# Performance work log

Measured on AMD Instinct MI355X. Metric: run time of the kernel, lower is better.

## Reference

```python
import jax, jax.numpy as jnp
import numpy as np

B, S, D, H = 8, 2048, 768, 12

def setup_inputs() -> dict:
    key = jax.random.key(0)
    kx, km, kk, kq, kv = jax.random.split(key, 5)
    return {
        "x": jax.random.normal(kx, (B, S, D), dtype=jnp.float32),
        "mask": jax.random.randint(km, (B, 1, S), 0, 2, dtype=jnp.int32),
        "key_weight": jax.random.normal(kk, (D, H), dtype=jnp.float32),
        "query_weight": jax.random.normal(kq, (D, H), dtype=jnp.float32),
        "value_weight": jax.random.normal(kv, (D, H), dtype=jnp.float32),
    }

def reference(x, mask, key_weight, query_weight, value_weight):
    scale = 1.0 / (key_weight.shape[-1] ** 0.5)
    k = jnp.einsum('bsd,dh->bsh', x, key_weight)
    q = jnp.einsum('bsd,dh->bsh', x, query_weight)
    v = jnp.einsum('bsd,dh->bsh', x, value_weight)
    # scores: (B, S, T) — full score matrix as in the original
    scores = jnp.einsum('bsh,bth->bst', q, k) * scale
    scores = jnp.where(mask == 0, -jnp.inf, scores)
    attn = jax.nn.softmax(scores, axis=-1)
    return jnp.einsum('bst,bth->bsh', attn, v)
```

## Files before the change

kernel.cpp:

```cpp
#include <hip/hip_runtime.h>
#include <math.h>

#define QSCALE (0.2886751345948129f * 1.4426950408889634f)

#if __has_builtin(__builtin_amdgcn_exp2f)
#define EXP2F(x) __builtin_amdgcn_exp2f(x)
#else
#define EXP2F(x) exp2f(x)
#endif

typedef __attribute__((ext_vector_type(8))) _Float16 half8;
typedef __attribute__((ext_vector_type(4))) _Float16 half4_t;
typedef __attribute__((ext_vector_type(4))) float floatx4;
typedef __attribute__((ext_vector_type(2))) unsigned int uint2v;

#define MFMA32F16(a, b, c) __builtin_amdgcn_mfma_f32_16x16x32_f16((a), (b), (c), 0, 0, 0)
#define MFMA16F16(a, b, c) __builtin_amdgcn_mfma_f32_16x16x16f16((a), (b), (c), 0, 0, 0)

static __device__ inline float bperm(float v, int addr_bytes) {
    return __int_as_float(__builtin_amdgcn_ds_bpermute(addr_bytes, __float_as_int(v)));
}

static __device__ inline float xmax16(float v) {
#if __has_builtin(__builtin_amdgcn_permlane16_swap)
    unsigned int u = __float_as_uint(v);
    uint2v r = __builtin_amdgcn_permlane16_swap(u, u, false, false);
    return fmaxf(__uint_as_float(r[0]), __uint_as_float(r[1]));
#else
    return fmaxf(v, bperm(v, ((int)(threadIdx.x & 63) ^ 16) << 2));
#endif
}
static __device__ inline float xmax32(float v) {
#if __has_builtin(__builtin_amdgcn_permlane32_swap)
    unsigned int u = __float_as_uint(v);
    uint2v r = __builtin_amdgcn_permlane32_swap(u, u, false, false);
    return fmaxf(__uint_as_float(r[0]), __uint_as_float(r[1]));
#else
    return fmaxf(v, bperm(v, ((int)(threadIdx.x & 63) ^ 32) << 2));
#endif
}

__global__ __launch_bounds__(256)
void prep(const float* __restrict__ Wq, const float* __restrict__ Wk,
          const float* __restrict__ Wv, const int* __restrict__ mask,
          _Float16* __restrict__ wfh, _Float16* __restrict__ wfl,
          int* __restrict__ dst, int* __restrict__ nvalid)
{
    const int b = blockIdx.x;
    const int tid = threadIdx.x;
    if (b < 18) {
        int t = b * 256 + tid;
        if (t >= 4608) return;
        int lane = t & 63;
        int nt   = (t >> 6) % 3;
        int ks   = t / 192;
        const float* W = (nt == 0) ? Wq : (nt == 1) ? Wk : Wv;
        const float scale = (nt == 0) ? QSCALE : 1.0f;
        int col = lane & 15;
        int q8  = lane >> 4;
        half8 hi, lo;
        #pragma unroll
        for (int j = 0; j < 8; ++j) {
            int dim = ks * 32 + q8 * 8 + j;
            float f = (col < 12) ? W[dim * 12 + col] * scale : 0.0f;
            _Float16 h = (_Float16)f;
            hi[j] = h;
            lo[j] = (_Float16)(f - (float)h);
        }
        size_t off = ((size_t)(ks * 3 + nt) * 64 + lane) * 8;
        *(half8*)(wfh + off) = hi;
        *(half8*)(wfl + off) = lo;
    } else {
        __shared__ int cnt[256];
        const int bb = b - 18;
        const int* mb = mask + bb * 2048;
        int local[8]; int c = 0;
        #pragma unroll
        for (int i = 0; i < 8; ++i) { local[i] = (mb[tid * 8 + i] != 0); c += local[i]; }
        cnt[tid] = c;
        __syncthreads();
        for (int off = 1; off < 256; off <<= 1) {
            int u = cnt[tid];
            int add = (tid >= off) ? cnt[tid - off] : 0;
            __syncthreads();
            cnt[tid] = u + add;
            __syncthreads();
        }
        int run = (tid == 0) ? 0 : cnt[tid - 1];
        int* db = dst + bb * 2048;
        #pragma unroll
        for (int i = 0; i < 8; ++i) { db[tid * 8 + i] = local[i] ? run : -1; run += local[i]; }
        if (tid == 255) nvalid[bb] = cnt[255];
    }
}

__global__ __launch_bounds__(256, 3)
void qkv_mfma(const float* __restrict__ x, const _Float16* __restrict__ wfh,
              const _Float16* __restrict__ wfl, const int* __restrict__ dst,
              _Float16* __restrict__ qA, _Float16* __restrict__ qB,
              _Float16* __restrict__ kfp, _Float16* __restrict__ vtf)
{
    __shared__ __align__(16) float cbuf[3072];
    const int tid  = threadIdx.x;
    const int lane = tid & 63;
    const int w    = tid >> 6;
    const int g    = blockIdx.x;
    const int rowbase = g * 16;
    const int m15 = lane & 15;
    const int q8  = lane >> 4;

    const float* xbase = x + (size_t)(rowbase + m15) * 768 + q8 * 8;
    const half8* WH = (const half8*)wfh;
    const half8* WL = (const half8*)wfl;

    float xv[6][8];
    #pragma unroll
    for (int s = 0; s < 6; ++s) {
        const int ks = w * 6 + s;
        *(float4*)(xv[s])     = *(const float4*)(xbase + ks * 32);
        *(float4*)(xv[s] + 4) = *(const float4*)(xbase + ks * 32 + 4);
    }

    floatx4 acc0 = {0.f, 0.f, 0.f, 0.f};
    floatx4 acc1 = acc0, acc2 = acc0;

    half8 bh[2][3], bl[2][3];
    {
        const int ks = w * 6;
        #pragma unroll
        for (int n = 0; n < 3; ++n) {
            bh[0][n] = WH[(ks * 3 + n) * 64 + lane];
            bl[0][n] = WL[(ks * 3 + n) * 64 + lane];
        }
    }

    #pragma unroll
    for (int s = 0; s < 6; ++s) {
        const int cur = s & 1, nxt = cur ^ 1;
        if (s < 5) {
            const int ksn = w * 6 + s + 1;
            #pragma unroll
            for (int n = 0; n < 3; ++n) {
                bh[nxt][n] = WH[(ksn * 3 + n) * 64 + lane];
                bl[nxt][n] = WL[(ksn * 3 + n) * 64 + lane];
            }
        }
        half8 ah, al;
        #pragma unroll
        for (int j = 0; j < 8; ++j) {
            _Float16 h = (_Float16)xv[s][j];
            ah[j] = h;
            al[j] = (_Float16)(xv[s][j] - (float)h);
        }
        acc0 = MFMA32F16(ah, bh[cur][0], acc0);
        acc1 = MFMA32F16(ah, bh[cur][1], acc1);
        acc2 = MFMA32F16(ah, bh[cur][2], acc2);
        acc0 = MFMA32F16(al, bh[cur][0], acc0);
        acc1 = MFMA32F16(al, bh[cur][1], acc1);
        acc2 = MFMA32F16(al, bh[cur][2], acc2);
        acc0 = MFMA32F16(ah, bl[cur][0], acc0);
        acc1 = MFMA32F16(ah, bl[cur][1], acc1);
        acc2 = MFMA32F16(ah, bl[cur][2], acc2);
    }

    *(floatx4*)(cbuf + ((w * 3 + 0) * 64 + lane) * 4) = acc0;
    *(floatx4*)(cbuf + ((w * 3 + 1) * 64 + lane) * 4) = acc1;
    *(floatx4*)(cbuf + ((w * 3 + 2) * 64 + lane) * 4) = acc2;
    __syncthreads();
    if (w < 3) {
        floatx4 t0 = *(const floatx4*)(cbuf + ((0 * 3 + w) * 64 + lane) * 4);
        floatx4 t1 = *(const floatx4*)(cbuf + ((1 * 3 + w) * 64 + lane) * 4);
        floatx4 t2 = *(const floatx4*)(cbuf + ((2 * 3 + w) * 64 + lane) * 4);
        floatx4 t3 = *(const floatx4*)(cbuf + ((3 * 3 + w) * 64 + lane) * 4);
        floatx4 tot = t0 + t1 + t2 + t3;
        const int col = m15;
        const int r0  = q8 * 4;
        #pragma unroll
        for (int r = 0; r < 4; ++r) {
            const int row = rowbase + r0 + r;
            const float val = tot[r];
            if (w == 0) {
                if (col < 12) {
                    size_t fb = (size_t)g * 64;
                    size_t offL = (fb + (col >> 3) * 16 + (r0 + r)) * 8 + (col & 7);
                    size_t offH = (fb + (2 + (col >> 3)) * 16 + (r0 + r)) * 8 + (col & 7);
                    _Float16 h = (_Float16)val;
                    qA[offL] = h;
                    qA[offH] = h;
                    qB[offL] = (_Float16)(val - (float)h);
                    qB[offH] = (_Float16)0.0f;
                }
            } else {
                const int d = dst[row];
                if (d >= 0) {
                    const int bb = row >> 11;
                    if (w == 1) {
                        size_t fb = ((size_t)(bb * 128 + (d >> 4))) * 64;
                        size_t offH = (fb + (col >> 3) * 16 + (d & 15)) * 8 + (col & 7);
                        size_t offL = (fb + (2 + (col >> 3)) * 16 + (d & 15)) * 8 + (col & 7);
                        if (col < 12) {
                            _Float16 h = (_Float16)val;
                            kfp[offH] = h;
                            kfp[offL] = (_Float16)(val - (float)h);
                        } else {
                            kfp[offH] = (_Float16)0.0f;
                            kfp[offL] = (_Float16)0.0f;
                        }
                    } else {
                        if (col < 12) {
                            size_t off = (((size_t)(bb * 128 + (d >> 4))) * 64
                                          + ((d & 15) >> 2) * 16 + col) * 4 + (d & 3);
                            vtf[off] = (_Float16)val;
                        } else if (col == 12) {
                            size_t off = (((size_t)(bb * 128 + (d >> 4))) * 64
                                          + ((d & 15) >> 2) * 16 + 12) * 4 + (d & 3);
                            vtf[off] = (_Float16)1.0f;
                        }
                    }
                }
            }
        }
    }
}

__global__ __launch_bounds__(256)
void attn(const _Float16* __restrict__ qAf, const _Float16* __restrict__ qBf,
          const _Float16* __restrict__ kfp, const _Float16* __restrict__ vtf,
          const int* __restrict__ nvalid, float* __restrict__ out)
{
    __shared__ float cm[256];
    __shared__ __align__(16) floatx4 co[256];
    const int tid  = threadIdx.x;
    const int lane = tid & 63;
    const int w    = tid >> 6;
    const int bb   = blockIdx.x & 7;
    const int gl   = blockIdx.x >> 3;
    const int g0   = bb * 128 + gl;
    const int m15  = lane & 15;

    const half8 qA0 = *(const half8*)(qAf + ((size_t)g0 * 64 + lane) * 8);
    const half8 qB0 = *(const half8*)(qBf + ((size_t)g0 * 64 + lane) * 8);

    const half8* KP = (const half8*)kfp + (size_t)bb * 128 * 64;
    const half4_t* VT = (const half4_t*)vtf + (size_t)bb * 128 * 64;

    const int nv = nvalid[bb];
    const int nt = (nv + 15) >> 4;

    float m0 = -INFINITY;
    floatx4 o0 = {0.f, 0.f, 0.f, 0.f};

    int t = w;
    half8 kp, kp2;
    half4_t va, va2;
    if (t < nt)     { kp  = KP[t * 64 + lane];       va  = VT[t * 64 + lane]; }
    if (t + 4 < nt) { kp2 = KP[(t + 4) * 64 + lane]; va2 = VT[(t + 4) * 64 + lane]; }
    for (; t < nt; t += 8) {
        const int t2 = t + 4;
        const bool has2 = (t2 < nt);
        half8 nkp, nkp2; half4_t nva, nva2;
        if (t + 8 < nt)  { nkp  = KP[(t + 8) * 64 + lane];  nva  = VT[(t + 8) * 64 + lane]; }
        if (t + 12 < nt) { nkp2 = KP[(t + 12) * 64 + lane]; nva2 = VT[(t + 12) * 64 + lane]; }
        if (t == nt - 1) {
            const int kb = t * 16;
            if (kb + m15 >= nv) {
                #pragma unroll
                for (int j = 0; j < 8; ++j) kp[j] = (_Float16)0.0f;
            }
            const int kv = kb + (lane >> 4) * 4;
            #pragma unroll
            for (int j = 0; j < 4; ++j)
                if (kv + j >= nv) va[j] = (_Float16)0.0f;
        }
        if (has2 && t2 == nt - 1) {
            const int kb = t2 * 16;
            if (kb + m15 >= nv) {
                #pragma unroll
                for (int j = 0; j < 8; ++j) kp2[j] = (_Float16)0.0f;
            }
            const int kv = kb + (lane >> 4) * 4;
            #pragma unroll
            for (int j = 0; j < 4; ++j)
                if (kv + j >= nv) va2[j] = (_Float16)0.0f;
        }
        const floatx4 z = {0.f, 0.f, 0.f, 0.f};
        floatx4 s0a = MFMA32F16(kp, qA0, z);
        floatx4 s0b = MFMA32F16(kp, qB0, z);
        floatx4 s1 = z;
        if (has2) {
            floatx4 s1a = MFMA32F16(kp2, qA0, z);
            floatx4 s1b = MFMA32F16(kp2, qB0, z);
            s1 = s1a + s1b;
        }
        floatx4 s0 = s0a + s0b;
        float pm = fmaxf(fmaxf(s0.x, s0.y), fmaxf(s0.z, s0.w));
        if (has2) {
            float pm1 = fmaxf(fmaxf(s1.x, s1.y), fmaxf(s1.z, s1.w));
            pm = fmaxf(pm, pm1);
        }
        pm = xmax16(pm);
        pm = xmax32(pm);
        float mref;
        if (__all(pm <= m0)) {
            mref = m0;
        } else {
            float mnew = fmaxf(m0, pm);
            float corr = EXP2F(m0 - mnew);
            o0.x *= corr; o0.y *= corr; o0.z *= corr; o0.w *= corr;
            m0 = mnew; mref = mnew;
        }
        half4_t pb;
        pb[0] = (_Float16)EXP2F(s0.x - mref);
        pb[1] = (_Float16)EXP2F(s0.y - mref);
        pb[2] = (_Float16)EXP2F(s0.z - mref);
        pb[3] = (_Float16)EXP2F(s0.w - mref);
        o0 = MFMA16F16(va, pb, o0);
        if (has2) {
            half4_t pb2;
            pb2[0] = (_Float16)EXP2F(s1.x - mref);
            pb2[1] = (_Float16)EXP2F(s1.y - mref);
            pb2[2] = (_Float16)EXP2F(s1.z - mref);
            pb2[3] = (_Float16)EXP2F(s1.w - mref);
            o0 = MFMA16F16(va2, pb2, o0);
        }
        kp = nkp; va = nva; kp2 = nkp2; va2 = nva2;
    }

    cm[w * 64 + lane] = m0;
    co[w * 64 + lane] = o0;
    __syncthreads();
    if (w == 0) {
        float gm = -INFINITY;
        #pragma unroll
        for (int w2 = 0; w2 < 4; ++w2) gm = fmaxf(gm, cm[w2 * 64 + lane]);
        floatx4 O = {0.f, 0.f, 0.f, 0.f};
        #pragma unroll
        for (int w2 = 0; w2 < 4; ++w2) {
            float f = EXP2F(cm[w2 * 64 + lane] - gm);
            floatx4 ow = co[w2 * 64 + lane];
            O.x += ow.x * f; O.y += ow.y * f; O.z += ow.z * f; O.w += ow.w * f;
        }
        float L = bperm(O.x, (48 + m15) << 2);
        float inv = 1.0f / L;
        if ((lane >> 4) < 3) {
            float4 ov = make_float4(O.x * inv, O.y * inv, O.z * inv, O.w * inv);
            *(float4*)(out + ((size_t)g0 * 16 + m15) * 12 + (lane >> 4) * 4) = ov;
        }
    }
}

extern "C" void kernel_launch(void* const* d_in, const int* in_sizes, int n_in,
                              void* d_out, int out_size, void* d_ws, size_t ws_size,
                              hipStream_t stream) {
    const float* x    = (const float*)d_in[0];
    const int*   mask = (const int*)  d_in[1];
    const float* Wk   = (const float*)d_in[2];
    const float* Wq   = (const float*)d_in[3];
    const float* Wv   = (const float*)d_in[4];
    float* out = (float*)d_out;

    char* base = (char*)d_ws;
    _Float16* qA  = (_Float16*)(base);
    _Float16* qB  = (_Float16*)(base + (1u << 20));
    _Float16* kfp = (_Float16*)(base + (2u << 20));
    _Float16* vtf = (_Float16*)(base + (3u << 20));
    _Float16* wfh = (_Float16*)(base + 3670016);
    _Float16* wfl = (_Float16*)(base + 3670016 + 73728);
    int* dst      = (int*)(base + 3817472);
    int* nvalid   = (int*)(base + 3817472 + 65536);

    prep<<<26, 256, 0, stream>>>(Wq, Wk, Wv, mask, wfh, wfl, dst, nvalid);
    qkv_mfma<<<1024, 256, 0, stream>>>(x, wfh, wfl, dst, qA, qB, kfp, vtf);
    attn<<<1024, 256, 0, stream>>>(qA, qB, kfp, vtf, nvalid, out);
}
```

Before: 108.4 us.

## Fuse weight split and mask prefix scan into QKV projection kernel

Removes the separate prep launch. Each QKV block now converts the fp32 weights to hi/lo fp16 fragments itself, and recomputes the mask prefix scan for its batch into shared memory. This saves one kernel launch and the global round trip for the dst indices. In exchange, all 1024 blocks redo the weight conversion with strided scalar loads, and each redoes a 2048-element scan with many barriers.

```diff
diff --git a/kernel.cpp b/kernel.cpp
--- a/kernel.cpp
+++ b/kernel.cpp
@@ -40,39 +40,94 @@
 #endif
 }
 
-__global__ __launch_bounds__(256)
-void prep(const float* __restrict__ Wq, const float* __restrict__ Wk,
-          const float* __restrict__ Wv, const int* __restrict__ mask,
-          _Float16* __restrict__ wfh, _Float16* __restrict__ wfl,
-          int* __restrict__ dst, int* __restrict__ nvalid)
+__global__ __launch_bounds__(256, 3)
+void qkv_mfma(const float* __restrict__ x, const float* __restrict__ Wq,
+              const float* __restrict__ Wk, const float* __restrict__ Wv,
+              const int* __restrict__ mask,
+              _Float16* __restrict__ qA, _Float16* __restrict__ qB,
+              _Float16* __restrict__ kfp, _Float16* __restrict__ vtf,
+              int* __restrict__ nvalid)
 {
-    const int b = blockIdx.x;
-    const int tid = threadIdx.x;
-    if (b < 18) {
-        int t = b * 256 + tid;
-        if (t >= 4608) return;
-        int lane = t & 63;
-        int nt   = (t >> 6) % 3;
-        int ks   = t / 192;
-        const float* W = (nt == 0) ? Wq : (nt == 1) ? Wk : Wv;
-        const float scale = (nt == 0) ? QSCALE : 1.0f;
-        int col = lane & 15;
-        int q8  = lane >> 4;
-        half8 hi, lo;
+    __shared__ __align__(16) float cbuf[3072];
+    const int tid  = threadIdx.x;
+    const int lane = tid & 63;
+    const int w    = tid >> 6;
+    const int g    = blockIdx.x;
+    const int rowbase = g * 16;
+    const int bb   = g >> 7;
+    const int m15  = lane & 15;
+    const int q8   = lane >> 4;
+
+    const float* xbase = x + (size_t)(rowbase + m15) * 768 + q8 * 8;
+
+    float xv[6][8];
+    #pragma unroll
+    for (int s = 0; s < 6; ++s) {
+        const int ks = w * 6 + s;
+        *(float4*)(xv[s])     = *(const float4*)(xbase + ks * 32);
+        *(float4*)(xv[s] + 4) = *(const float4*)(xbase + ks * 32 + 4);
+    }
+
+    floatx4 acc0 = {0.f, 0.f, 0.f, 0.f};
+    floatx4 acc1 = acc0, acc2 = acc0;
+
+    #pragma unroll
+    for (int s = 0; s < 6; ++s) {
+        const int ks = w * 6 + s;
+        float wf0[8], wf1[8], wf2[8];
         #pragma unroll
         for (int j = 0; j < 8; ++j) {
-            int dim = ks * 32 + q8 * 8 + j;
-            float f = (col < 12) ? W[dim * 12 + col] * scale : 0.0f;
-            _Float16 h = (_Float16)f;
-            hi[j] = h;
-            lo[j] = (_Float16)(f - (float)h);
-        }
-        size_t off = ((size_t)(ks * 3 + nt) * 64 + lane) * 8;
-        *(half8*)(wfh + off) = hi;
-        *(half8*)(wfl + off) = lo;
-    } else {
-        __shared__ int cnt[256];
-        const int bb = b - 18;
+            const int dim = ks * 32 + q8 * 8 + j;
+            const bool ok = (m15 < 12);
+            wf0[j] = ok ? Wq[dim * 12 + m15] * QSCALE : 0.0f;
+            wf1[j] = ok ? Wk[dim * 12 + m15] : 0.0f;
+            wf2[j] = ok ? Wv[dim * 12 + m15] : 0.0f;
+        }
+        half8 bh0, bh1, bh2, bl0, bl1, bl2;
+        #pragma unroll
+        for (int j = 0; j < 8; ++j) {
+            _Float16 h0 = (_Float16)wf0[j];
+            _Float16 h1 = (_Float16)wf1[j];
+            _Float16 h2 = (_Float16)wf2[j];
+            bh0[j] = h0; bl0[j] = (_Float16)(wf0[j] - (float)h0);
+            bh1[j] = h1; bl1[j] = (_Float16)(wf1[j] - (float)h1);
+            bh2[j] = h2; bl2[j] = (_Float16)(wf2[j] - (float)h2);
+        }
+        half8 ah, al;
+        #pragma unroll
+        for (int j = 0; j < 8; ++j) {
+            _Float16 h = (_Float16)xv[s][j];
+            ah[j] = h;
+            al[j] = (_Float16)(xv[s][j] - (float)h);
+        }
+        acc0 = MFMA32F16(ah, bh0, acc0);
+        acc1 = MFMA32F16(ah, bh1, acc1);
+        acc2 = MFMA32F16(ah, bh2, acc2);
+        acc0 = MFMA32F16(al, bh0, acc0);
+        acc1 = MFMA32F16(al, bh1, acc1);
+        acc2 = MFMA32F16(al, bh2, acc2);
+        acc0 = MFMA32F16(ah, bl0, acc0);
+        acc1 = MFMA32F16(ah, bl1, acc1);
+        acc2 = MFMA32F16(ah, bl2, acc2);
+    }
+
+    *(floatx4*)(cbuf + ((w * 3 + 0) * 64 + lane) * 4) = acc0;
+    *(floatx4*)(cbuf + ((w * 3 + 1) * 64 + lane) * 4) = acc1;
+    *(floatx4*)(cbuf + ((w * 3 + 2) * 64 + lane) * 4) = acc2;
+    __syncthreads();
+    floatx4 tot = {0.f, 0.f, 0.f, 0.f};
+    if (w < 3) {
+        floatx4 t0 = *(const floatx4*)(cbuf + ((0 * 3 + w) * 64 + lane) * 4);
+        floatx4 t1 = *(const floatx4*)(cbuf + ((1 * 3 + w) * 64 + lane) * 4);
+        floatx4 t2 = *(const floatx4*)(cbuf + ((2 * 3 + w) * 64 + lane) * 4);
+        floatx4 t3 = *(const floatx4*)(cbuf + ((3 * 3 + w) * 64 + lane) * 4);
+        tot = t0 + t1 + t2 + t3;
+    }
+    __syncthreads();
+
+    {
+        int* cnt  = (int*)cbuf;
+        int* dstl = (int*)cbuf + 256;
         const int* mb = mask + bb * 2048;
         int local[8]; int c = 0;
         #pragma unroll
@@ -87,92 +142,14 @@
             __syncthreads();
         }
         int run = (tid == 0) ? 0 : cnt[tid - 1];
-        int* db = dst + bb * 2048;
-        #pragma unroll
-        for (int i = 0; i < 8; ++i) { db[tid * 8 + i] = local[i] ? run : -1; run += local[i]; }
+        #pragma unroll
+        for (int i = 0; i < 8; ++i) { dstl[tid * 8 + i] = local[i] ? run : -1; run += local[i]; }
         if (tid == 255) nvalid[bb] = cnt[255];
-    }
-}
-
-__global__ __launch_bounds__(256, 3)
-void qkv_mfma(const float* __restrict__ x, const _Float16* __restrict__ wfh,
-              const _Float16* __restrict__ wfl, const int* __restrict__ dst,
-              _Float16* __restrict__ qA, _Float16* __restrict__ qB,
-              _Float16* __restrict__ kfp, _Float16* __restrict__ vtf)
-{
-    __shared__ __align__(16) float cbuf[3072];
-    const int tid  = threadIdx.x;
-    const int lane = tid & 63;
-    const int w    = tid >> 6;
-    const int g    = blockIdx.x;
-    const int rowbase = g * 16;
-    const int m15 = lane & 15;
-    const int q8  = lane >> 4;
-
-    const float* xbase = x + (size_t)(rowbase + m15) * 768 + q8 * 8;
-    const half8* WH = (const half8*)wfh;
-    const half8* WL = (const half8*)wfl;
-
-    float xv[6][8];
-    #pragma unroll
-    for (int s = 0; s < 6; ++s) {
-        const int ks = w * 6 + s;
-        *(float4*)(xv[s])     = *(const float4*)(xbase + ks * 32);
-        *(float4*)(xv[s] + 4) = *(const float4*)(xbase + ks * 32 + 4);
-    }
-
-    floatx4 acc0 = {0.f, 0.f, 0.f, 0.f};
-    floatx4 acc1 = acc0, acc2 = acc0;
-
-    half8 bh[2][3], bl[2][3];
-    {
-        const int ks = w * 6;
-        #pragma unroll
-        for (int n = 0; n < 3; ++n) {
-            bh[0][n] = WH[(ks * 3 + n) * 64 + lane];
-            bl[0][n] = WL[(ks * 3 + n) * 64 + lane];
-        }
-    }
-
-    #pragma unroll
-    for (int s = 0; s < 6; ++s) {
-        const int cur = s & 1, nxt = cur ^ 1;
-        if (s < 5) {
-            const int ksn = w * 6 + s + 1;
-            #pragma unroll
-            for (int n = 0; n < 3; ++n) {
-                bh[nxt][n] = WH[(ksn * 3 + n) * 64 + lane];
-                bl[nxt][n] = WL[(ksn * 3 + n) * 64 + lane];
-            }
-        }
-        half8 ah, al;
-        #pragma unroll
-        for (int j = 0; j < 8; ++j) {
-            _Float16 h = (_Float16)xv[s][j];
-            ah[j] = h;
-            al[j] = (_Float16)(xv[s][j] - (float)h);
-        }
-        acc0 = MFMA32F16(ah, bh[cur][0], acc0);
-        acc1 = MFMA32F16(ah, bh[cur][1], acc1);
-        acc2 = MFMA32F16(ah, bh[cur][2], acc2);
-        acc0 = MFMA32F16(al, bh[cur][0], acc0);
-        acc1 = MFMA32F16(al, bh[cur][1], acc1);
-        acc2 = MFMA32F16(al, bh[cur][2], acc2);
-        acc0 = MFMA32F16(ah, bl[cur][0], acc0);
-        acc1 = MFMA32F16(ah, bl[cur][1], acc1);
-        acc2 = MFMA32F16(ah, bl[cur][2], acc2);
-    }
-
-    *(floatx4*)(cbuf + ((w * 3 + 0) * 64 + lane) * 4) = acc0;
-    *(floatx4*)(cbuf + ((w * 3 + 1) * 64 + lane) * 4) = acc1;
-    *(floatx4*)(cbuf + ((w * 3 + 2) * 64 + lane) * 4) = acc2;
-    __syncthreads();
+        __syncthreads();
+    }
+
     if (w < 3) {
-        floatx4 t0 = *(const floatx4*)(cbuf + ((0 * 3 + w) * 64 + lane) * 4);
-        floatx4 t1 = *(const floatx4*)(cbuf + ((1 * 3 + w) * 64 + lane) * 4);
-        floatx4 t2 = *(const floatx4*)(cbuf + ((2 * 3 + w) * 64 + lane) * 4);
-        floatx4 t3 = *(const floatx4*)(cbuf + ((3 * 3 + w) * 64 + lane) * 4);
-        floatx4 tot = t0 + t1 + t2 + t3;
+        const int* dstl = (const int*)cbuf + 256;
         const int col = m15;
         const int r0  = q8 * 4;
         #pragma unroll
@@ -191,9 +168,8 @@
                     qB[offH] = (_Float16)0.0f;
                 }
             } else {
-                const int d = dst[row];
+                const int d = dstl[row & 2047];
                 if (d >= 0) {
-                    const int bb = row >> 11;
                     if (w == 1) {
                         size_t fb = ((size_t)(bb * 128 + (d >> 4))) * 64;
                         size_t offH = (fb + (col >> 3) * 16 + (d & 15)) * 8 + (col & 7);
@@ -364,12 +340,8 @@
     _Float16* qB  = (_Float16*)(base + (1u << 20));
     _Float16* kfp = (_Float16*)(base + (2u << 20));
     _Float16* vtf = (_Float16*)(base + (3u << 20));
-    _Float16* wfh = (_Float16*)(base + 3670016);
-    _Float16* wfl = (_Float16*)(base + 3670016 + 73728);
-    int* dst      = (int*)(base + 3817472);
-    int* nvalid   = (int*)(base + 3817472 + 65536);
-
-    prep<<<26, 256, 0, stream>>>(Wq, Wk, Wv, mask, wfh, wfl, dst, nvalid);
-    qkv_mfma<<<1024, 256, 0, stream>>>(x, wfh, wfl, dst, qA, qB, kfp, vtf);
+    int* nvalid   = (int*)(base + 3670016);
+
+    qkv_mfma<<<1024, 256, 0, stream>>>(x, Wq, Wk, Wv, mask, qA, qB, kfp, vtf, nvalid);
     attn<<<1024, 256, 0, stream>>>(qA, qB, kfp, vtf, nvalid, out);
 }
```

Measured after the change: 116.9 us. 1.08x slower.
